# Kernel optimization log

Hardware: AMD Instinct MI355X
Metric: run time of the kernel (lower is better)

## Reference

```python
import jax, jax.numpy as jnp
import numpy as np

POOL_D, POOL_H, POOL_W = 4, 7, 7
SPATIAL_SCALE = 0.25
SAMPLING_RATIO = 2


def setup_inputs() -> dict:
    key = jax.random.key(0)
    k1, k2, k3, k4 = jax.random.split(key, 4)
    N, C, D, H, W = 2, 128, 32, 64, 64
    features = jax.random.normal(k1, (N, C, D, H, W), dtype=jnp.float32)
    R = 256
    inv = 1.0 / SPATIAL_SCALE  # rois live in image coords; features at stride 4
    batch = jax.random.randint(k2, (R,), 0, N).astype(jnp.float32)
    dims = jnp.array([D, H, W], dtype=jnp.float32)
    starts = jax.random.uniform(k3, (R, 3)) * dims * inv * 0.6
    sizes = (0.1 + 0.3 * jax.random.uniform(k4, (R, 3))) * dims * inv
    z1, y1, x1 = starts[:, 0], starts[:, 1], starts[:, 2]
    z2, y2, x2 = z1 + sizes[:, 0], y1 + sizes[:, 1], x1 + sizes[:, 2]
    # roi layout: (batch_idx, x1, y1, z1, x2, y2, z2)
    rois = jnp.stack([batch, x1, y1, z1, x2, y2, z2], axis=1).astype(jnp.float32)
    return {"features": features, "rois": rois}


def _axis(coords, size):
    # classic RoIAlign border handling: outside [-1, size] -> 0 contribution
    valid = (coords >= -1.0) & (coords <= float(size))
    c = jnp.clip(coords, 0.0, float(size) - 1.0)
    lo = jnp.floor(c)
    hi = jnp.minimum(lo + 1.0, float(size) - 1.0)
    w = c - lo  # weight of the hi corner
    return lo.astype(jnp.int32), hi.astype(jnp.int32), w, valid


def roi_align_3d(features, rois):
    N, C, D, H, W = features.shape
    R = rois.shape[0]
    sr = SAMPLING_RATIO
    b = rois[:, 0].astype(jnp.int32)
    x1 = rois[:, 1] * SPATIAL_SCALE
    y1 = rois[:, 2] * SPATIAL_SCALE
    z1 = rois[:, 3] * SPATIAL_SCALE
    x2 = rois[:, 4] * SPATIAL_SCALE
    y2 = rois[:, 5] * SPATIAL_SCALE
    z2 = rois[:, 6] * SPATIAL_SCALE
    rd = jnp.maximum(z2 - z1, 1.0)
    rh = jnp.maximum(y2 - y1, 1.0)
    rw = jnp.maximum(x2 - x1, 1.0)

    def sample_coords(start, extent, P):
        # sampling_ratio sample centers per output bin -> [R, P*sr]
        t = (jnp.arange(P * sr, dtype=jnp.float32) + 0.5) / sr
        return start[:, None] + t[None, :] * (extent / P)[:, None]

    zs = sample_coords(z1, rd, POOL_D)  # [R, SD]
    ys = sample_coords(y1, rh, POOL_H)  # [R, SH]
    xs = sample_coords(x1, rw, POOL_W)  # [R, SW]
    zlo, zhi, wz, vz = _axis(zs, D)
    ylo, yhi, wy, vy = _axis(ys, H)
    xlo, xhi, wx, vx = _axis(xs, W)

    B = b[:, None, None, None]
    Z = lambda a: a[:, :, None, None]
    Y = lambda a: a[:, None, :, None]
    X = lambda a: a[:, None, None, :]

    def g(zi, yi, xi):
        # gather -> [R, SD, SH, SW, C]
        return features[B, :, Z(zi), Y(yi), X(xi)]

    wz1, wy1, wx1 = Z(wz)[..., None], Y(wy)[..., None], X(wx)[..., None]
    wz0, wy0, wx0 = 1.0 - wz1, 1.0 - wy1, 1.0 - wx1
    val = (g(zlo, ylo, xlo) * (wz0 * wy0 * wx0)
           + g(zlo, ylo, xhi) * (wz0 * wy0 * wx1)
           + g(zlo, yhi, xlo) * (wz0 * wy1 * wx0)
           + g(zlo, yhi, xhi) * (wz0 * wy1 * wx1)
           + g(zhi, ylo, xlo) * (wz1 * wy0 * wx0)
           + g(zhi, ylo, xhi) * (wz1 * wy0 * wx1)
           + g(zhi, yhi, xlo) * (wz1 * wy1 * wx0)
           + g(zhi, yhi, xhi) * (wz1 * wy1 * wx1))
    valid = (Z(vz) & Y(vy) & X(vx))[..., None]
    val = jnp.where(valid, val, 0.0)
    # average the sr^3 samples per bin
    val = val.reshape(R, POOL_D, sr, POOL_H, sr, POOL_W, sr, C)
    out = val.mean(axis=(2, 4, 6))  # [R, PD, PH, PW, C]
    return jnp.transpose(out, (0, 4, 1, 2, 3))  # [R, C, PD, PH, PW]


def reference(features, rois):
    return roi_align_3d(features, rois)
```

## Files before the change

kernel.cpp:

```cpp
#include <hip/hip_runtime.h>

constexpr int C_  = 128;
constexpr int D_  = 32;
constexpr int H_  = 64;
constexpr int W_  = 64;
constexpr int PD = 4;
constexpr int PH = 7;
constexpr int PW = 7;
constexpr int SR = 2;
constexpr float SCALE = 0.25f;
constexpr int S_ = D_ * H_ * W_;
constexpr int BINS_PER_ROI = PD * PH * PW;
constexpr int SLAB = PH * PW;

__device__ __forceinline__ void axis2(float start, float extent, int P, int p,
                                      int size, int lo[2], int hi[2],
                                      float w[2], bool v[2]) {
    float bin = extent / (float)P;
#pragma unroll
    for (int u = 0; u < 2; ++u) {
        float t = ((float)(p * SR + u) + 0.5f) / (float)SR;
        float coord = start + t * bin;
        v[u] = (coord >= -1.0f) && (coord <= (float)size);
        float cc = fminf(fmaxf(coord, 0.0f), (float)size - 1.0f);
        float fl = floorf(cc);
        lo[u] = (int)fl;
        hi[u] = min(lo[u] + 1, size - 1);
        w[u] = cc - fl;
    }
}

__device__ __forceinline__ unsigned short f2bf(float f) {
    unsigned int u = __float_as_uint(f);
    u += 0x7fffu + ((u >> 16) & 1u);
    return (unsigned short)(u >> 16);
}

__device__ __forceinline__ float4 bf4(uint2 v) {
    float4 f;
    f.x = __uint_as_float(v.x << 16);
    f.y = __uint_as_float(v.x & 0xffff0000u);
    f.z = __uint_as_float(v.y << 16);
    f.w = __uint_as_float(v.y & 0xffff0000u);
    return f;
}

__global__ __launch_bounds__(256) void transpose_bf16(
    const float* __restrict__ in, unsigned short* __restrict__ outp) {
    __shared__ __align__(16) unsigned short tile[64][132];
    const int n  = blockIdx.y;
    const int s0 = blockIdx.x * 64;
    const int t  = threadIdx.x;

    const float* src = in + (size_t)n * C_ * S_;
    unsigned short* dst = outp + (size_t)n * C_ * S_;

    {
        const int cl = t >> 4;
        const int s4 = (t & 15) * 4;
#pragma unroll
        for (int p = 0; p < 8; ++p) {
            const int c = cl + 16 * p;
            const float4 v =
                *(const float4*)&src[(size_t)c * S_ + (s0 + s4)];
            tile[s4 + 0][c] = f2bf(v.x);
            tile[s4 + 1][c] = f2bf(v.y);
            tile[s4 + 2][c] = f2bf(v.z);
            tile[s4 + 3][c] = f2bf(v.w);
        }
    }
    __syncthreads();
    {
        const int sl = t >> 5;
        const int c4 = (t & 31) * 4;
#pragma unroll
        for (int p = 0; p < 8; ++p) {
            const int s = sl + 8 * p;
            const unsigned short a0 = tile[s][c4 + 0];
            const unsigned short a1 = tile[s][c4 + 1];
            const unsigned short a2 = tile[s][c4 + 2];
            const unsigned short a3 = tile[s][c4 + 3];
            uint2 v;
            v.x = (unsigned int)a0 | ((unsigned int)a1 << 16);
            v.y = (unsigned int)a2 | ((unsigned int)a3 << 16);
            *(uint2*)&dst[(size_t)(s0 + s) * C_ + c4] = v;
        }
    }
}

__global__ __launch_bounds__(256) void roi_align_slab(
    const unsigned short* __restrict__ ft,
    const float* __restrict__ rois,
    float* __restrict__ out,
    int R) {
    __shared__ __align__(16) float tile[SLAB][132];

    int r, pd;
    if ((R & 7) == 0) {
        const int xcd = blockIdx.x & 7;
        const int q = blockIdx.x >> 3;
        pd = q & 3;
        r = ((q >> 2) << 3) + xcd;
    } else {
        r = blockIdx.x >> 2;
        pd = blockIdx.x & 3;
    }

    const int t = threadIdx.x;
    const int grp = t >> 5;
    const int c4 = (t & 31) * 4;

    const float* roi = rois + (size_t)r * 7;
    const int b = (int)roi[0];
    const float x1 = roi[1] * SCALE, y1 = roi[2] * SCALE, z1 = roi[3] * SCALE;
    const float x2 = roi[4] * SCALE, y2 = roi[5] * SCALE, z2 = roi[6] * SCALE;
    const float rd = fmaxf(z2 - z1, 1.0f);
    const float rh = fmaxf(y2 - y1, 1.0f);
    const float rw = fmaxf(x2 - x1, 1.0f);

    int zlo[2], zhi[2];
    float wz[2];
    bool vz[2];
    axis2(z1, rd, PD, pd, D_, zlo, zhi, wz, vz);

#pragma unroll 1
    for (int k = 0; k < 7; ++k) {
        const int slot = grp + 8 * k;
        if (slot < SLAB) {
            const int ph = slot / PW;
            const int pw = slot - ph * PW;

            int ylo[2], yhi[2], xlo[2], xhi[2];
            float wy[2], wx[2];
            bool vy[2], vx[2];
            axis2(y1, rh, PH, ph, H_, ylo, yhi, wy, vy);
            axis2(x1, rw, PW, pw, W_, xlo, xhi, wx, vx);

            float4 acc = make_float4(0.f, 0.f, 0.f, 0.f);
#pragma unroll
            for (int i = 0; i < 2; ++i) {
                if (!vz[i]) continue;
                const float wz1 = wz[i], wz0 = 1.0f - wz1;
#pragma unroll
                for (int j = 0; j < 2; ++j) {
                    if (!vy[j]) continue;
                    const float wy1 = wy[j], wy0 = 1.0f - wy1;
                    const size_t r00 =
                        (((size_t)b * D_ + zlo[i]) * H_ + ylo[j]) * W_;
                    const size_t r10 =
                        (((size_t)b * D_ + zhi[i]) * H_ + ylo[j]) * W_;
                    const size_t r01 =
                        (((size_t)b * D_ + zlo[i]) * H_ + yhi[j]) * W_;
                    const size_t r11 =
                        (((size_t)b * D_ + zhi[i]) * H_ + yhi[j]) * W_;
#pragma unroll
                    for (int kk = 0; kk < 2; ++kk) {
                        if (!vx[kk]) continue;
                        const float wx1 = wx[kk], wx0 = 1.0f - wx1;
                        const size_t xl = xlo[kk], xh = xhi[kk];
                        const float4 f000 =
                            bf4(*(const uint2*)&ft[(r00 + xl) * C_ + c4]);
                        const float4 f001 =
                            bf4(*(const uint2*)&ft[(r00 + xh) * C_ + c4]);
                        const float4 f010 =
                            bf4(*(const uint2*)&ft[(r01 + xl) * C_ + c4]);
                        const float4 f011 =
                            bf4(*(const uint2*)&ft[(r01 + xh) * C_ + c4]);
                        const float4 f100 =
                            bf4(*(const uint2*)&ft[(r10 + xl) * C_ + c4]);
                        const float4 f101 =
                            bf4(*(const uint2*)&ft[(r10 + xh) * C_ + c4]);
                        const float4 f110 =
                            bf4(*(const uint2*)&ft[(r11 + xl) * C_ + c4]);
                        const float4 f111 =
                            bf4(*(const uint2*)&ft[(r11 + xh) * C_ + c4]);
                        const float w000 = wz0 * wy0 * wx0,
                                    w001 = wz0 * wy0 * wx1;
                        const float w010 = wz0 * wy1 * wx0,
                                    w011 = wz0 * wy1 * wx1;
                        const float w100 = wz1 * wy0 * wx0,
                                    w101 = wz1 * wy0 * wx1;
                        const float w110 = wz1 * wy1 * wx0,
                                    w111 = wz1 * wy1 * wx1;
                        acc.x += w000 * f000.x + w001 * f001.x +
                                 w010 * f010.x + w011 * f011.x +
                                 w100 * f100.x + w101 * f101.x +
                                 w110 * f110.x + w111 * f111.x;
                        acc.y += w000 * f000.y + w001 * f001.y +
                                 w010 * f010.y + w011 * f011.y +
                                 w100 * f100.y + w101 * f101.y +
                                 w110 * f110.y + w111 * f111.y;
                        acc.z += w000 * f000.z + w001 * f001.z +
                                 w010 * f010.z + w011 * f011.z +
                                 w100 * f100.z + w101 * f101.z +
                                 w110 * f110.z + w111 * f111.z;
                        acc.w += w000 * f000.w + w001 * f001.w +
                                 w010 * f010.w + w011 * f011.w +
                                 w100 * f100.w + w101 * f101.w +
                                 w110 * f110.w + w111 * f111.w;
                    }
                }
            }
            const float s = 1.0f / (SR * SR * SR);
            acc.x *= s; acc.y *= s; acc.z *= s; acc.w *= s;
            *(float4*)&tile[slot][c4] = acc;
        }
    }

    __syncthreads();

    const size_t obase = (size_t)r * C_ * BINS_PER_ROI + (size_t)pd * SLAB;
#pragma unroll 1
    for (int idx = t; idx < C_ * SLAB; idx += 256) {
        const int c = idx / SLAB;
        const int o = idx - c * SLAB;
        out[obase + (size_t)c * BINS_PER_ROI + o] = tile[o][c];
    }
}

__global__ void roi_align_direct(const float* __restrict__ feat,
                                 const float* __restrict__ rois,
                                 float* __restrict__ out, int total) {
    const int tid = blockIdx.x * blockDim.x + threadIdx.x;
    if (tid >= total) return;
    int t = tid;
    const int pw = t % PW; t /= PW;
    const int ph = t % PH; t /= PH;
    const int pd = t % PD; t /= PD;
    const int c = t % C_;  t /= C_;
    const int r = t;

    const float* roi = rois + (size_t)r * 7;
    const int b = (int)roi[0];
    const float x1 = roi[1] * SCALE, y1 = roi[2] * SCALE, z1 = roi[3] * SCALE;
    const float x2 = roi[4] * SCALE, y2 = roi[5] * SCALE, z2 = roi[6] * SCALE;
    const float rd = fmaxf(z2 - z1, 1.0f);
    const float rh = fmaxf(y2 - y1, 1.0f);
    const float rw = fmaxf(x2 - x1, 1.0f);

    int zlo[2], zhi[2], ylo[2], yhi[2], xlo[2], xhi[2];
    float wz[2], wy[2], wx[2];
    bool vz[2], vy[2], vx[2];
    axis2(z1, rd, PD, pd, D_, zlo, zhi, wz, vz);
    axis2(y1, rh, PH, ph, H_, ylo, yhi, wy, vy);
    axis2(x1, rw, PW, pw, W_, xlo, xhi, wx, vx);

    const float* fc = feat + ((size_t)b * C_ + c) * S_;
    float acc = 0.0f;
#pragma unroll
    for (int i = 0; i < 2; ++i) {
        if (!vz[i]) continue;
#pragma unroll
        for (int j = 0; j < 2; ++j) {
            if (!vy[j]) continue;
            const size_t r00 = ((size_t)zlo[i] * H_ + ylo[j]) * W_;
            const size_t r10 = ((size_t)zhi[i] * H_ + ylo[j]) * W_;
            const size_t r01 = ((size_t)zlo[i] * H_ + yhi[j]) * W_;
            const size_t r11 = ((size_t)zhi[i] * H_ + yhi[j]) * W_;
            const float wz1 = wz[i], wz0 = 1.0f - wz1;
            const float wy1 = wy[j], wy0 = 1.0f - wy1;
#pragma unroll
            for (int k = 0; k < 2; ++k) {
                if (!vx[k]) continue;
                const float wx1 = wx[k], wx0 = 1.0f - wx1;
                acc += wz0 * (wy0 * (wx0 * fc[r00 + xlo[k]] + wx1 * fc[r00 + xhi[k]]) +
                              wy1 * (wx0 * fc[r01 + xlo[k]] + wx1 * fc[r01 + xhi[k]])) +
                       wz1 * (wy0 * (wx0 * fc[r10 + xlo[k]] + wx1 * fc[r10 + xhi[k]]) +
                              wy1 * (wx0 * fc[r11 + xlo[k]] + wx1 * fc[r11 + xhi[k]]));
            }
        }
    }
    out[tid] = acc * (1.0f / (SR * SR * SR));
}

extern "C" void kernel_launch(void* const* d_in, const int* in_sizes, int n_in,
                              void* d_out, int out_size, void* d_ws,
                              size_t ws_size, hipStream_t stream) {
    const float* features = (const float*)d_in[0];
    const float* rois = (const float*)d_in[1];
    float* out = (float*)d_out;

    const int R = in_sizes[1] / 7;
    const int N = in_sizes[0] / (C_ * S_);
    const size_t need = (size_t)in_sizes[0] * sizeof(unsigned short);

    if (ws_size >= need) {
        unsigned short* ft = (unsigned short*)d_ws;

        dim3 tg(S_ / 64, N);
        transpose_bf16<<<tg, 256, 0, stream>>>(features, ft);

        roi_align_slab<<<R * PD, 256, 0, stream>>>(ft, rois, out, R);
    } else {
        const int total = R * C_ * BINS_PER_ROI;
        roi_align_direct<<<(total + 255) / 256, 256, 0, stream>>>(
            features, rois, out, total);
    }
}
```

Baseline: 270.6 us.

## Pack bf16 pairs in transpose LDS tile, double slab block size, nontemporal stores

The transpose kernel now packs two channels' bf16 values into one 32-bit word in shared memory. This uses a padded uint tile to cut LDS bank conflicts and halves the number of shared-memory reads on the write-out side. The slab kernel moves from 256 to 512 threads per block, so each block runs 16 groups and needs 4 iterations over the 49 bins instead of 7. Output writes become nontemporal stores to avoid polluting the cache. The larger block may lower occupancy and raise register pressure.

```diff
diff --git a/kernel.cpp b/kernel.cpp
--- a/kernel.cpp
+++ b/kernel.cpp
@@ -30,10 +30,10 @@
     }
 }
 
-__device__ __forceinline__ unsigned short f2bf(float f) {
+__device__ __forceinline__ unsigned int f2bf(float f) {
     unsigned int u = __float_as_uint(f);
     u += 0x7fffu + ((u >> 16) & 1u);
-    return (unsigned short)(u >> 16);
+    return u >> 16;
 }
 
 __device__ __forceinline__ float4 bf4(uint2 v) {
@@ -46,49 +46,47 @@
 }
 
 __global__ __launch_bounds__(256) void transpose_bf16(
-    const float* __restrict__ in, unsigned short* __restrict__ outp) {
-    __shared__ __align__(16) unsigned short tile[64][132];
+    const float* __restrict__ in, unsigned int* __restrict__ outp) {
+    __shared__ unsigned int tileu[64][67];
     const int n  = blockIdx.y;
     const int s0 = blockIdx.x * 64;
     const int t  = threadIdx.x;
 
     const float* src = in + (size_t)n * C_ * S_;
-    unsigned short* dst = outp + (size_t)n * C_ * S_;
+    unsigned int* dst = outp + (size_t)n * (C_ / 2) * S_;
 
     {
-        const int cl = t >> 4;
-        const int s4 = (t & 15) * 4;
-#pragma unroll
-        for (int p = 0; p < 8; ++p) {
-            const int c = cl + 16 * p;
-            const float4 v =
-                *(const float4*)&src[(size_t)c * S_ + (s0 + s4)];
-            tile[s4 + 0][c] = f2bf(v.x);
-            tile[s4 + 1][c] = f2bf(v.y);
-            tile[s4 + 2][c] = f2bf(v.z);
-            tile[s4 + 3][c] = f2bf(v.w);
+        const int cp0 = t >> 4;
+        const int s4  = (t & 15) * 4;
+#pragma unroll
+        for (int p = 0; p < 4; ++p) {
+            const int cp = cp0 + 16 * p;
+            const int c = cp * 2;
+            const float4 a = *(const float4*)&src[(size_t)c * S_ + (s0 + s4)];
+            const float4 b =
+                *(const float4*)&src[(size_t)(c + 1) * S_ + (s0 + s4)];
+            tileu[s4 + 0][cp] = f2bf(a.x) | (f2bf(b.x) << 16);
+            tileu[s4 + 1][cp] = f2bf(a.y) | (f2bf(b.y) << 16);
+            tileu[s4 + 2][cp] = f2bf(a.z) | (f2bf(b.z) << 16);
+            tileu[s4 + 3][cp] = f2bf(a.w) | (f2bf(b.w) << 16);
         }
     }
     __syncthreads();
     {
-        const int sl = t >> 5;
-        const int c4 = (t & 31) * 4;
+        const int sl  = t >> 5;
+        const int cp2 = (t & 31) * 2;
 #pragma unroll
         for (int p = 0; p < 8; ++p) {
             const int s = sl + 8 * p;
-            const unsigned short a0 = tile[s][c4 + 0];
-            const unsigned short a1 = tile[s][c4 + 1];
-            const unsigned short a2 = tile[s][c4 + 2];
-            const unsigned short a3 = tile[s][c4 + 3];
             uint2 v;
-            v.x = (unsigned int)a0 | ((unsigned int)a1 << 16);
-            v.y = (unsigned int)a2 | ((unsigned int)a3 << 16);
-            *(uint2*)&dst[(size_t)(s0 + s) * C_ + c4] = v;
-        }
-    }
-}
-
-__global__ __launch_bounds__(256) void roi_align_slab(
+            v.x = tileu[s][cp2 + 0];
+            v.y = tileu[s][cp2 + 1];
+            *(uint2*)&dst[(size_t)(s0 + s) * (C_ / 2) + cp2] = v;
+        }
+    }
+}
+
+__global__ __launch_bounds__(512) void roi_align_slab(
     const unsigned short* __restrict__ ft,
     const float* __restrict__ rois,
     float* __restrict__ out,
@@ -124,8 +122,8 @@
     axis2(z1, rd, PD, pd, D_, zlo, zhi, wz, vz);
 
 #pragma unroll 1
-    for (int k = 0; k < 7; ++k) {
-        const int slot = grp + 8 * k;
+    for (int k = 0; k < 4; ++k) {
+        const int slot = grp + 16 * k;
         if (slot < SLAB) {
             const int ph = slot / PW;
             const int pw = slot - ph * PW;
@@ -211,10 +209,11 @@
 
     const size_t obase = (size_t)r * C_ * BINS_PER_ROI + (size_t)pd * SLAB;
 #pragma unroll 1
-    for (int idx = t; idx < C_ * SLAB; idx += 256) {
+    for (int idx = t; idx < C_ * SLAB; idx += 512) {
         const int c = idx / SLAB;
         const int o = idx - c * SLAB;
-        out[obase + (size_t)c * BINS_PER_ROI + o] = tile[o][c];
+        __builtin_nontemporal_store(tile[o][c],
+                                    &out[obase + (size_t)c * BINS_PER_ROI + o]);
     }
 }
 
@@ -288,9 +287,9 @@
         unsigned short* ft = (unsigned short*)d_ws;
 
         dim3 tg(S_ / 64, N);
-        transpose_bf16<<<tg, 256, 0, stream>>>(features, ft);
-
-        roi_align_slab<<<R * PD, 256, 0, stream>>>(ft, rois, out, R);
+        transpose_bf16<<<tg, 256, 0, stream>>>(features, (unsigned int*)ft);
+
+        roi_align_slab<<<R * PD, 512, 0, stream>>>(ft, rois, out, R);
     } else {
         const int total = R * C_ * BINS_PER_ROI;
         roi_align_direct<<<(total + 255) / 256, 256, 0, stream>>>(
```

After: 268.0 us. Within noise of the previous version (-1.0%).
